# Kernel optimization log

Measured on AMD Instinct MI355X. Metric: run time of the kernel, lower is better.

Reference implementation:

```python
import jax, jax.numpy as jnp
import numpy as np

N, M, D = 8192, 8192, 64


def setup_inputs() -> dict:
    key = jax.random.key(0)
    kx, ky, kg = jax.random.split(key, 3)
    x = jax.random.normal(kx, (N, D), dtype=jnp.float32)
    y = jax.random.normal(ky, (M, D), dtype=jnp.float32)
    # per-dimension gamma (anisotropic branch: gamma.numel() == d), positive
    gamma = jax.random.uniform(kg, (D,), dtype=jnp.float32, minval=0.1, maxval=2.0)
    return {"x": x, "y": y, "gamma": gamma}


def reference(x, y, gamma):
    # k(x, y) = exp(-sum_i gamma_i * (x_i - y_i)^2)
    # Fused form: gamma-weighted squared distance via the expansion
    # avoids materializing the (n, m, d) broadcast tensor.
    sq_x = jnp.sum(gamma * x * x, axis=-1)          # (n,)
    sq_y = jnp.sum(gamma * y * y, axis=-1)          # (m,)
    cross = jnp.einsum('nd,md->nm', x, gamma * y)   # (n, m)
    norm = sq_x[:, None] + sq_y[None, :] - 2.0 * cross
    return jnp.exp(-norm)
```

## Files before the change

### kernel.cpp

```cpp
#include <hip/hip_runtime.h>
#include <hip/hip_bf16.h>
#include <stdint.h>


#define KPAD 136
#define CSTRIDE 68

typedef __attribute__((ext_vector_type(8))) short bfrag8;
typedef __attribute__((ext_vector_type(4))) float facc4;
typedef __attribute__((ext_vector_type(4))) float f32x4;

__device__ __forceinline__ unsigned short f2bf(float v) {
  uint32_t u = __float_as_uint(v);
  u += 0x7fffu + ((u >> 16) & 1u);
  return (unsigned short)(u >> 16);
}
__device__ __forceinline__ float bf2f(unsigned short h) {
  return __uint_as_float(((uint32_t)h) << 16);
}

__global__ __launch_bounds__(256)
void qkm_prep(const float* __restrict__ x, const float* __restrict__ y,
              const float* __restrict__ gamma,
              unsigned short* __restrict__ Apack, unsigned short* __restrict__ Bpack,
              float* __restrict__ sqx, float* __restrict__ sqy, int N, int M) {
  const int t = blockIdx.x * blockDim.x + threadIdx.x;
  const bool isB = (t >= N);
  const int r = isB ? (t - N) : t;
  if (isB && r >= M) return;
  const float4* src = (const float4*)((isB ? y : x) + (size_t)r * 64);
  const float4* gv = (const float4*)gamma;
  unsigned short* dst = isB ? Bpack : Apack;

  unsigned short hi[64], lo[64];
  float s = 0.f;
#pragma unroll
  for (int c = 0; c < 16; ++c) {
    const float4 v = src[c];
    const float4 g4 = gv[c];
    const float vj[4] = {v.x, v.y, v.z, v.w};
    const float gj[4] = {g4.x, g4.y, g4.z, g4.w};
#pragma unroll
    for (int j = 0; j < 4; ++j) {
      const float val = vj[j];
      s = fmaf(gj[j] * val, val, s);
      const float wv = isB ? (2.f * gj[j] * val) : val;
      const unsigned short h = f2bf(wv);
      hi[c * 4 + j] = h;
      lo[c * 4 + j] = f2bf(wv - bf2f(h));
    }
  }
  (isB ? sqy : sqx)[r] = s;

  const int p = r >> 4, lr = r & 15;
#pragma unroll
  for (int kb = 0; kb < 4; ++kb) {
#pragma unroll
    for (int lq = 0; lq < 4; ++lq) {
      unsigned short tmp[8];
#pragma unroll
      for (int j = 0; j < 8; ++j) {
        const int kk = kb * 32 + lq * 8 + j;
        tmp[j] = (kk < 64) ? hi[kk] : lo[kk - 64];
      }
      uint4 pk;
      pk.x = (uint32_t)tmp[0] | ((uint32_t)tmp[1] << 16);
      pk.y = (uint32_t)tmp[2] | ((uint32_t)tmp[3] << 16);
      pk.z = (uint32_t)tmp[4] | ((uint32_t)tmp[5] << 16);
      pk.w = (uint32_t)tmp[6] | ((uint32_t)tmp[7] << 16);
      *(uint4*)&dst[(((size_t)(p * 4 + kb)) * 64 + lq * 16 + lr) * 8] = pk;
    }
  }
}

__global__ __launch_bounds__(256, 4)
void qkm_main(const unsigned short* __restrict__ Apack,
              const unsigned short* __restrict__ Bpack,
              const float* __restrict__ sqx, const float* __restrict__ sqy,
              float* __restrict__ out, int M) {
  __shared__ __align__(16) float Ct[64 * CSTRIDE];

  const int tid = threadIdx.x;
  const int l = tid & 63, wv = tid >> 6;
  const int n0 = blockIdx.y * 64, m0 = blockIdx.x * 64;
  const int lr = l & 15, lq = l >> 4;

  const unsigned short* Af = Apack + (((size_t)((n0 >> 4) + wv) * 4) * 64 + l) * 8;
  const unsigned short* Bf = Bpack + (((size_t)(m0 >> 4) * 4) * 64 + l) * 8;

  facc4 acc[4] = {};
  bfrag8 aH[2], aT[2], bT[4][2];

#pragma unroll
  for (int k = 0; k < 2; ++k) aH[k] = *(const bfrag8*)(Af + (size_t)k * 512);
#pragma unroll
  for (int ct = 0; ct < 4; ++ct)
#pragma unroll
    for (int k = 0; k < 2; ++k)
      bT[ct][k] = *(const bfrag8*)(Bf + ((size_t)ct * 4 + k) * 512);
#pragma unroll
  for (int k = 0; k < 2; ++k)
#pragma unroll
    for (int ct = 0; ct < 4; ++ct)
      acc[ct] = __builtin_amdgcn_mfma_f32_16x16x32_bf16(aH[k], bT[ct][k], acc[ct], 0, 0, 0);

#pragma unroll
  for (int k = 0; k < 2; ++k) aT[k] = *(const bfrag8*)(Af + (size_t)(2 + k) * 512);
#pragma unroll
  for (int k = 0; k < 2; ++k)
#pragma unroll
    for (int ct = 0; ct < 4; ++ct)
      acc[ct] = __builtin_amdgcn_mfma_f32_16x16x32_bf16(aT[k], bT[ct][k], acc[ct], 0, 0, 0);

#pragma unroll
  for (int ct = 0; ct < 4; ++ct)
#pragma unroll
    for (int k = 0; k < 2; ++k)
      bT[ct][k] = *(const bfrag8*)(Bf + ((size_t)ct * 4 + 2 + k) * 512);
#pragma unroll
  for (int k = 0; k < 2; ++k)
#pragma unroll
    for (int ct = 0; ct < 4; ++ct)
      acc[ct] = __builtin_amdgcn_mfma_f32_16x16x32_bf16(aH[k], bT[ct][k], acc[ct], 0, 0, 0);

  float* Ctw = Ct + wv * 16 * CSTRIDE;
  const float4 sx = *(const float4*)&sqx[n0 + wv * 16 + lq * 4];
  const float sxa[4] = {sx.x, sx.y, sx.z, sx.w};
#pragma unroll
  for (int ct = 0; ct < 4; ++ct) {
    const int col = ct * 16 + lr;
    const float sy = sqy[m0 + col];
#pragma unroll
    for (int q = 0; q < 4; ++q)
      Ctw[(lq * 4 + q) * CSTRIDE + col] = __expf(acc[ct][q] - sxa[q] - sy);
  }
#pragma unroll
  for (int i = 0; i < 4; ++i) {
    const int f = l + 64 * i;
    const int row = f >> 4;
    const int c4 = f & 15;
    const f32x4 v = *(const f32x4*)(Ctw + row * CSTRIDE + c4 * 4);
    __builtin_nontemporal_store(
        v, (f32x4*)(out + (size_t)(n0 + wv * 16 + row) * M + m0 + c4 * 4));
  }
}

__global__ __launch_bounds__(256, 4)
void qkm_rbf_fallback(const float* __restrict__ x, const float* __restrict__ y,
                      const float* __restrict__ gamma, float* __restrict__ out,
                      int M) {
  __shared__ __align__(16) unsigned short Ah[64 * KPAD];
  __shared__ __align__(16) unsigned short Bh[64 * KPAD];
  __shared__ float sqx[64];
  __shared__ float sqy[64];

  const int tid = threadIdx.x;
  const int n0 = blockIdx.y * 64;
  const int m0 = blockIdx.x * 64;
  {
    const float4* xv = (const float4*)(x + (size_t)n0 * 64);
    const float4* yv = (const float4*)(y + (size_t)m0 * 64);
    const float4* gv = (const float4*)gamma;
#pragma unroll
    for (int i = 0; i < 4; ++i) {
      const int f = tid + 256 * i;
      const int r = f >> 4;
      const int c = f & 15;
      const float4 g4 = gv[c];
      const float gj[4] = {g4.x, g4.y, g4.z, g4.w};
      {
        const float4 v = xv[f];
        const float vj[4] = {v.x, v.y, v.z, v.w};
        unsigned short h[4], lo[4];
        float s = 0.f;
#pragma unroll
        for (int j = 0; j < 4; ++j) {
          const float xval = vj[j];
          h[j] = f2bf(xval);
          lo[j] = f2bf(xval - bf2f(h[j]));
          s = fmaf(gj[j] * xval, xval, s);
        }
        uint2 hp, lp;
        hp.x = (uint32_t)h[0] | ((uint32_t)h[1] << 16);
        hp.y = (uint32_t)h[2] | ((uint32_t)h[3] << 16);
        lp.x = (uint32_t)lo[0] | ((uint32_t)lo[1] << 16);
        lp.y = (uint32_t)lo[2] | ((uint32_t)lo[3] << 16);
        *(uint2*)&Ah[r * KPAD + c * 4]      = hp;
        *(uint2*)&Ah[r * KPAD + 64 + c * 4] = lp;
        s += __shfl_xor(s, 1); s += __shfl_xor(s, 2);
        s += __shfl_xor(s, 4); s += __shfl_xor(s, 8);
        if (c == 0) sqx[r] = s;
      }
      {
        const float4 v = yv[f];
        const float vj[4] = {v.x, v.y, v.z, v.w};
        unsigned short h[4], lo[4];
        float s = 0.f;
#pragma unroll
        for (int j = 0; j < 4; ++j) {
          const float yval = vj[j];
          const float w = 2.f * gj[j] * yval;
          h[j] = f2bf(w);
          lo[j] = f2bf(w - bf2f(h[j]));
          s = fmaf(gj[j] * yval, yval, s);
        }
        uint2 hp, lp;
        hp.x = (uint32_t)h[0] | ((uint32_t)h[1] << 16);
        hp.y = (uint32_t)h[2] | ((uint32_t)h[3] << 16);
        lp.x = (uint32_t)lo[0] | ((uint32_t)lo[1] << 16);
        lp.y = (uint32_t)lo[2] | ((uint32_t)lo[3] << 16);
        *(uint2*)&Bh[r * KPAD + c * 4]      = hp;
        *(uint2*)&Bh[r * KPAD + 64 + c * 4] = lp;
        s += __shfl_xor(s, 1); s += __shfl_xor(s, 2);
        s += __shfl_xor(s, 4); s += __shfl_xor(s, 8);
        if (c == 0) sqy[r] = s;
      }
    }
  }
  __syncthreads();

  const int l = tid & 63;
  const int wv = tid >> 6;
  const int rb = (wv & 1) * 32;
  const int cb = (wv >> 1) * 32;
  const int lr = l & 15;
  const int lq = l >> 4;

  facc4 acc[2][2] = {};
  const unsigned short* A0 = &Ah[(rb + lr) * KPAD + lq * 8];
  const unsigned short* A1 = A0 + 16 * KPAD;
  const unsigned short* B0 = &Bh[(cb + lr) * KPAD + lq * 8];
  const unsigned short* B1 = B0 + 16 * KPAD;
  const int akb[6] = {0, 32, 0, 32, 64, 96};
  const int bkb[6] = {0, 32, 64, 96, 0, 32};
#pragma unroll
  for (int p = 0; p < 6; ++p) {
    bfrag8 a0 = *(const bfrag8*)(A0 + akb[p]);
    bfrag8 a1 = *(const bfrag8*)(A1 + akb[p]);
    bfrag8 b0 = *(const bfrag8*)(B0 + bkb[p]);
    bfrag8 b1 = *(const bfrag8*)(B1 + bkb[p]);
    acc[0][0] = __builtin_amdgcn_mfma_f32_16x16x32_bf16(a0, b0, acc[0][0], 0, 0, 0);
    acc[0][1] = __builtin_amdgcn_mfma_f32_16x16x32_bf16(a0, b1, acc[0][1], 0, 0, 0);
    acc[1][0] = __builtin_amdgcn_mfma_f32_16x16x32_bf16(a1, b0, acc[1][0], 0, 0, 0);
    acc[1][1] = __builtin_amdgcn_mfma_f32_16x16x32_bf16(a1, b1, acc[1][1], 0, 0, 0);
  }
  __syncthreads();

  float* Ct = (float*)Ah;
  const float sy0 = sqy[cb + lr];
  const float sy1 = sqy[cb + 16 + lr];
#pragma unroll
  for (int ti = 0; ti < 2; ++ti) {
    const int rloc = rb + ti * 16 + lq * 4;
    const float4 sx = *(const float4*)&sqx[rloc];
    const float sxa[4] = {sx.x, sx.y, sx.z, sx.w};
#pragma unroll
    for (int q = 0; q < 4; ++q) {
      float* crow = Ct + (size_t)(rloc + q) * CSTRIDE;
      crow[cb + lr]      = __expf(acc[ti][0][q] - sxa[q] - sy0);
      crow[cb + 16 + lr] = __expf(acc[ti][1][q] - sxa[q] - sy1);
    }
  }
  __syncthreads();
#pragma unroll
  for (int i = 0; i < 4; ++i) {
    const int f = tid + 256 * i;
    const int row = f >> 4;
    const int c4 = f & 15;
    const float4 v = *(const float4*)(Ct + row * CSTRIDE + c4 * 4);
    *(float4*)(out + (size_t)(n0 + row) * M + m0 + c4 * 4) = v;
  }
}

extern "C" void kernel_launch(void* const* d_in, const int* in_sizes, int n_in,
                              void* d_out, int out_size, void* d_ws, size_t ws_size,
                              hipStream_t stream) {
  const float* x = (const float*)d_in[0];
  const float* y = (const float*)d_in[1];
  const float* g = (const float*)d_in[2];
  float* out = (float*)d_out;
  const int D = in_sizes[2];
  const int N = in_sizes[0] / D;
  const int M = in_sizes[1] / D;

  const size_t aBytes = (size_t)N * 128 * sizeof(unsigned short);
  const size_t bBytes = (size_t)M * 128 * sizeof(unsigned short);
  const size_t sxBytes = (size_t)N * sizeof(float);
  const size_t syBytes = (size_t)M * sizeof(float);
  const size_t need = aBytes + bBytes + sxBytes + syBytes + 256;

  if (ws_size >= need) {
    char* ws = (char*)d_ws;
    unsigned short* Apack = (unsigned short*)ws;
    unsigned short* Bpack = (unsigned short*)(ws + aBytes);
    float* sqx = (float*)(ws + aBytes + bBytes);
    float* sqy = (float*)(ws + aBytes + bBytes + sxBytes);
    qkm_prep<<<(N + M + 255) / 256, 256, 0, stream>>>(x, y, g, Apack, Bpack, sqx, sqy, N, M);
    dim3 grid(M / 64, N / 64);
    qkm_main<<<grid, dim3(256), 0, stream>>>(Apack, Bpack, sqx, sqy, out, M);
  } else {
    dim3 grid(M / 64, N / 64);
    qkm_rbf_fallback<<<grid, dim3(256), 0, stream>>>(x, y, g, out, M);
  }
}
```

Measured before the change: 280.3 us.

## Enlarge main kernel tile to 128x128 with 32 rows per wave

```diff
diff --git a/kernel.cpp b/kernel.cpp
--- a/kernel.cpp
+++ b/kernel.cpp
@@ -5,6 +5,7 @@
 
 #define KPAD 136
 #define CSTRIDE 68
+#define CS2 128
 
 typedef __attribute__((ext_vector_type(8))) short bfrag8;
 typedef __attribute__((ext_vector_type(4))) float facc4;
@@ -73,75 +74,71 @@
   }
 }
 
-__global__ __launch_bounds__(256, 4)
+__global__ __launch_bounds__(256, 2)
 void qkm_main(const unsigned short* __restrict__ Apack,
               const unsigned short* __restrict__ Bpack,
               const float* __restrict__ sqx, const float* __restrict__ sqy,
               float* __restrict__ out, int M) {
-  __shared__ __align__(16) float Ct[64 * CSTRIDE];
+  __shared__ __align__(16) float Ct[128 * CS2];
 
   const int tid = threadIdx.x;
   const int l = tid & 63, wv = tid >> 6;
-  const int n0 = blockIdx.y * 64, m0 = blockIdx.x * 64;
+  const int n0 = blockIdx.y * 128, m0 = blockIdx.x * 128;
   const int lr = l & 15, lq = l >> 4;
 
-  const unsigned short* Af = Apack + (((size_t)((n0 >> 4) + wv) * 4) * 64 + l) * 8;
+  const unsigned short* Af = Apack + (((size_t)((n0 >> 4) + wv * 2) * 4) * 64 + l) * 8;
   const unsigned short* Bf = Bpack + (((size_t)(m0 >> 4) * 4) * 64 + l) * 8;
 
-  facc4 acc[4] = {};
-  bfrag8 aH[2], aT[2], bT[4][2];
-
-#pragma unroll
-  for (int k = 0; k < 2; ++k) aH[k] = *(const bfrag8*)(Af + (size_t)k * 512);
-#pragma unroll
-  for (int ct = 0; ct < 4; ++ct)
+  bfrag8 aH[2][2], aL[2][2];
+#pragma unroll
+  for (int rp = 0; rp < 2; ++rp)
+#pragma unroll
+    for (int k = 0; k < 2; ++k) {
+      aH[rp][k] = *(const bfrag8*)(Af + ((size_t)(rp * 4 + k)) * 512);
+      aL[rp][k] = *(const bfrag8*)(Af + ((size_t)(rp * 4 + 2 + k)) * 512);
+    }
+
+  facc4 acc[2][8] = {};
+#pragma unroll
+  for (int ct = 0; ct < 8; ++ct) {
+    bfrag8 bH[2], bL[2];
+#pragma unroll
+    for (int k = 0; k < 2; ++k) {
+      bH[k] = *(const bfrag8*)(Bf + ((size_t)(ct * 4 + k)) * 512);
+      bL[k] = *(const bfrag8*)(Bf + ((size_t)(ct * 4 + 2 + k)) * 512);
+    }
 #pragma unroll
     for (int k = 0; k < 2; ++k)
-      bT[ct][k] = *(const bfrag8*)(Bf + ((size_t)ct * 4 + k) * 512);
-#pragma unroll
-  for (int k = 0; k < 2; ++k)
-#pragma unroll
-    for (int ct = 0; ct < 4; ++ct)
-      acc[ct] = __builtin_amdgcn_mfma_f32_16x16x32_bf16(aH[k], bT[ct][k], acc[ct], 0, 0, 0);
-
-#pragma unroll
-  for (int k = 0; k < 2; ++k) aT[k] = *(const bfrag8*)(Af + (size_t)(2 + k) * 512);
-#pragma unroll
-  for (int k = 0; k < 2; ++k)
-#pragma unroll
-    for (int ct = 0; ct < 4; ++ct)
-      acc[ct] = __builtin_amdgcn_mfma_f32_16x16x32_bf16(aT[k], bT[ct][k], acc[ct], 0, 0, 0);
-
-#pragma unroll
-  for (int ct = 0; ct < 4; ++ct)
-#pragma unroll
-    for (int k = 0; k < 2; ++k)
-      bT[ct][k] = *(const bfrag8*)(Bf + ((size_t)ct * 4 + 2 + k) * 512);
-#pragma unroll
-  for (int k = 0; k < 2; ++k)
-#pragma unroll
-    for (int ct = 0; ct < 4; ++ct)
-      acc[ct] = __builtin_amdgcn_mfma_f32_16x16x32_bf16(aH[k], bT[ct][k], acc[ct], 0, 0, 0);
-
-  float* Ctw = Ct + wv * 16 * CSTRIDE;
-  const float4 sx = *(const float4*)&sqx[n0 + wv * 16 + lq * 4];
-  const float sxa[4] = {sx.x, sx.y, sx.z, sx.w};
-#pragma unroll
-  for (int ct = 0; ct < 4; ++ct) {
-    const int col = ct * 16 + lr;
-    const float sy = sqy[m0 + col];
-#pragma unroll
-    for (int q = 0; q < 4; ++q)
-      Ctw[(lq * 4 + q) * CSTRIDE + col] = __expf(acc[ct][q] - sxa[q] - sy);
-  }
-#pragma unroll
-  for (int i = 0; i < 4; ++i) {
+#pragma unroll
+      for (int rp = 0; rp < 2; ++rp) {
+        acc[rp][ct] = __builtin_amdgcn_mfma_f32_16x16x32_bf16(aH[rp][k], bH[k], acc[rp][ct], 0, 0, 0);
+        acc[rp][ct] = __builtin_amdgcn_mfma_f32_16x16x32_bf16(aL[rp][k], bH[k], acc[rp][ct], 0, 0, 0);
+        acc[rp][ct] = __builtin_amdgcn_mfma_f32_16x16x32_bf16(aH[rp][k], bL[k], acc[rp][ct], 0, 0, 0);
+      }
+  }
+
+  float* Cw = &Ct[wv * 32 * CS2];
+#pragma unroll
+  for (int rp = 0; rp < 2; ++rp) {
+    const float4 sx = *(const float4*)&sqx[n0 + wv * 32 + rp * 16 + lq * 4];
+    const float sxa[4] = {sx.x, sx.y, sx.z, sx.w};
+#pragma unroll
+    for (int ct = 0; ct < 8; ++ct) {
+      const int col = ct * 16 + lr;
+      const float sy = sqy[m0 + col];
+#pragma unroll
+      for (int q = 0; q < 4; ++q)
+        Cw[(rp * 16 + lq * 4 + q) * CS2 + col] = __expf(acc[rp][ct][q] - sxa[q] - sy);
+    }
+  }
+#pragma unroll
+  for (int i = 0; i < 16; ++i) {
     const int f = l + 64 * i;
-    const int row = f >> 4;
-    const int c4 = f & 15;
-    const f32x4 v = *(const f32x4*)(Ctw + row * CSTRIDE + c4 * 4);
+    const int row = f >> 5;
+    const int c4 = f & 31;
+    const f32x4 v = *(const f32x4*)(Cw + row * CS2 + c4 * 4);
     __builtin_nontemporal_store(
-        v, (f32x4*)(out + (size_t)(n0 + wv * 16 + row) * M + m0 + c4 * 4));
+        v, (f32x4*)(out + (size_t)(n0 + wv * 32 + row) * M + m0 + c4 * 4));
   }
 }
 
@@ -246,7 +243,7 @@
   }
   __syncthreads();
 
-  float* Ct = (float*)Ah;
+  float* Ctf = (float*)Ah;
   const float sy0 = sqy[cb + lr];
   const float sy1 = sqy[cb + 16 + lr];
 #pragma unroll
@@ -256,7 +253,7 @@
     const float sxa[4] = {sx.x, sx.y, sx.z, sx.w};
 #pragma unroll
     for (int q = 0; q < 4; ++q) {
-      float* crow = Ct + (size_t)(rloc + q) * CSTRIDE;
+      float* crow = Ctf + (size_t)(rloc + q) * CSTRIDE;
       crow[cb + lr]      = __expf(acc[ti][0][q] - sxa[q] - sy0);
       crow[cb + 16 + lr] = __expf(acc[ti][1][q] - sxa[q] - sy1);
     }
@@ -267,7 +264,7 @@
     const int f = tid + 256 * i;
     const int row = f >> 4;
     const int c4 = f & 15;
-    const float4 v = *(const float4*)(Ct + row * CSTRIDE + c4 * 4);
+    const float4 v = *(const float4*)(Ctf + row * CSTRIDE + c4 * 4);
     *(float4*)(out + (size_t)(n0 + row) * M + m0 + c4 * 4) = v;
   }
 }
@@ -296,7 +293,7 @@
     float* sqx = (float*)(ws + aBytes + bBytes);
     float* sqy = (float*)(ws + aBytes + bBytes + sxBytes);
     qkm_prep<<<(N + M + 255) / 256, 256, 0, stream>>>(x, y, g, Apack, Bpack, sqx, sqy, N, M);
-    dim3 grid(M / 64, N / 64);
+    dim3 grid(M / 128, N / 128);
     qkm_main<<<grid, dim3(256), 0, stream>>>(Apack, Bpack, sqx, sqy, out, M);
   } else {
     dim3 grid(M / 64, N / 64);
```

Result: no change. 285.7 us (+1.9%).
